# Performance work log

Hardware: AMD Instinct MI355X
Metric: run time of the kernel (lower is better)

The kernel has to match this reference:

```python
import jax, jax.numpy as jnp
import numpy as np

OUT = 7          # output_size
SR = 2           # sampling_ratio
IMG = 512.0      # image size (512, 512)
CANON_SCALE = 224.0
CANON_LVL = 4.0
LVL_MIN, LVL_MAX = 2, 6  # strides 4..64


def roi_align_level(feat, rois, scale):
    """torchvision roi_align (aligned=False) for all rois on one level.
    feat: [B,C,H,W], rois: [B,N,4] in image coords. Returns [B,N,C,7,7]."""
    B, C, H, W = feat.shape
    N = rois.shape[1]
    x1 = rois[..., 0] * scale
    y1 = rois[..., 1] * scale
    x2 = rois[..., 2] * scale
    y2 = rois[..., 3] * scale
    roi_w = jnp.maximum(x2 - x1, 1.0)
    roi_h = jnp.maximum(y2 - y1, 1.0)
    bin_w = roi_w / OUT
    bin_h = roi_h / OUT
    # 14 sample coordinates per axis: 7 bins x 2 samples, offset (i+0.5)/2 within bin
    grid = (jnp.arange(OUT, dtype=feat.dtype)[:, None]
            + (jnp.arange(SR, dtype=feat.dtype)[None, :] + 0.5) / SR).reshape(-1)  # [14]
    py = y1[..., None] + grid * bin_h[..., None]   # [B,N,14]
    px = x1[..., None] + grid * bin_w[..., None]   # [B,N,14]
    yy = py[..., :, None]                          # [B,N,14,1]
    xx = px[..., None, :]                          # [B,N,1,14]
    valid = (yy >= -1.0) & (yy <= H) & (xx >= -1.0) & (xx <= W)  # [B,N,14,14]
    y = jnp.clip(yy, 0.0, H - 1)
    x = jnp.clip(xx, 0.0, W - 1)
    y0f = jnp.floor(y)
    x0f = jnp.floor(x)
    ly = y - y0f   # [B,N,14,1]
    lx = x - x0f   # [B,N,1,14]
    y0 = y0f.astype(jnp.int32)
    x0 = x0f.astype(jnp.int32)
    y1i = jnp.minimum(y0 + 1, H - 1)
    x1i = jnp.minimum(x0 + 1, W - 1)

    flat = feat.reshape(B, C, H * W)

    def gather(yi, xi):
        idx = (yi * W + xi).reshape(B, -1)                     # [B, N*14*14]
        g = jax.vmap(lambda f, i: f[:, i])(flat, idx)          # [B, C, N*14*14]
        return g.reshape(B, C, N, SR * OUT, SR * OUT)

    w00 = ((1 - ly) * (1 - lx))[:, None]  # [B,1,N,14,14]
    w01 = ((1 - ly) * lx)[:, None]
    w10 = (ly * (1 - lx))[:, None]
    w11 = (ly * lx)[:, None]
    val = (gather(y0, x0) * w00 + gather(y0, x1i) * w01
           + gather(y1i, x0) * w10 + gather(y1i, x1i) * w11)
    val = val * valid[:, None].astype(feat.dtype)
    # average the SRxSR samples within each bin
    out = val.reshape(B, C, N, OUT, SR, OUT, SR).mean(axis=(4, 6))  # [B,C,N,7,7]
    return out.transpose(0, 2, 1, 3, 4)  # [B,N,C,7,7]


def setup_inputs() -> dict:
    key = jax.random.key(0)
    ks = jax.random.split(key, 6)
    B, C, N = 4, 256, 256
    feats = {}
    for lvl, hw in enumerate([128, 64, 32, 16, 8]):
        feats[f"feat{lvl}"] = jax.random.normal(ks[lvl], (B, C, hw, hw), dtype=jnp.float32)
    # random boxes inside the 512x512 image with x2>x1, y2>y1
    xy = jax.random.uniform(ks[5], (B, N, 2, 2), minval=0.0, maxval=IMG)
    lo = xy.min(axis=2)
    hi = xy.max(axis=2)
    rois = jnp.concatenate([lo, hi], axis=-1)  # [B,N,4] = (x1,y1,x2,y2)
    feats["rois"] = rois
    return feats


def reference(feat0, feat1, feat2, feat3, feat4, rois):
    B, N = rois.shape[0], rois.shape[1]
    feats = [feat0, feat1, feat2, feat3, feat4]
    scales = [0.25, 0.125, 0.0625, 0.03125, 0.015625]  # inferred from 128..8 vs 512
    # FPN level assignment (torchvision LevelMapper)
    area = (rois[..., 2] - rois[..., 0]) * (rois[..., 3] - rois[..., 1])
    lvl = jnp.floor(CANON_LVL + jnp.log2(jnp.sqrt(area) / CANON_SCALE + 1e-6))
    lvl = (jnp.clip(lvl, LVL_MIN, LVL_MAX) - LVL_MIN).astype(jnp.int32)  # [B,N] in 0..4
    # pool every roi on every level, then select its assigned level
    stacked = jnp.stack([roi_align_level(f, rois, s) for f, s in zip(feats, scales)],
                        axis=2)  # [B,N,5,C,7,7]
    sel = jnp.take_along_axis(stacked,
                              lvl[:, :, None, None, None, None].astype(jnp.int32),
                              axis=2)[:, :, 0]  # [B,N,C,7,7]
    B_, N_, C, _, _ = sel.shape
    return sel.reshape(B_ * N_, C, OUT, OUT)
```

## Files before the change

### kernel.cpp

```cpp
#include <hip/hip_runtime.h>

#define OUT 7
#define NB 4
#define NC 256
#define NN 256
#define EPR (NC * OUT * OUT)

typedef float nfloat4 __attribute__((ext_vector_type(4)));

__global__ __launch_bounds__(256) void transpose_all(
    const float* __restrict__ f0, const float* __restrict__ f1,
    const float* __restrict__ f2, const float* __restrict__ f3,
    const float* __restrict__ f4, float* __restrict__ T)
{
    __shared__ float tile[32][33];
    const int bx = blockIdx.x;

    const float* in; float* outp; int P, t, shp;
    if (bx < 16384)      { in = f0; outp = T;            P = 16384; t = bx;         shp = 9; }
    else if (bx < 20480) { in = f1; outp = T + 16777216; P = 4096;  t = bx - 16384; shp = 7; }
    else if (bx < 21504) { in = f2; outp = T + 20971520; P = 1024;  t = bx - 20480; shp = 5; }
    else if (bx < 21760) { in = f3; outp = T + 22020096; P = 256;   t = bx - 21504; shp = 3; }
    else                 { in = f4; outp = T + 22282240; P = 64;    t = bx - 21760; shp = 1; }

    const int pt   = t & ((1 << shp) - 1);
    const int rest = t >> shp;
    const int ct   = rest & 7;
    const int b    = rest >> 3;
    const int p0   = pt << 5;
    const int c0   = ct << 5;
    const int tx   = threadIdx.x & 7;
    const int ty   = threadIdx.x >> 3;

    const float* src = in + ((size_t)((b << 8) + c0 + ty)) * P + p0 + (tx << 2);
    nfloat4 v = *(const nfloat4*)src;
    tile[ty][tx * 4 + 0] = v.x;
    tile[ty][tx * 4 + 1] = v.y;
    tile[ty][tx * 4 + 2] = v.z;
    tile[ty][tx * 4 + 3] = v.w;
    __syncthreads();

    nfloat4 w;
    w.x = tile[4 * tx + 0][ty];
    w.y = tile[4 * tx + 1][ty];
    w.z = tile[4 * tx + 2][ty];
    w.w = tile[4 * tx + 3][ty];
    float* dst = outp + ((size_t)b * P + p0 + ty) * NC + c0 + (tx << 2);
    *(nfloat4*)dst = w;
}

__global__ __launch_bounds__(256, 3) void msroi_fast(
    const float* __restrict__ T, const float* __restrict__ rois,
    float* __restrict__ out)
{
    const int roi = blockIdx.x;
    const int tid = threadIdx.x;

    __shared__ float s_wyt[14], s_wyb[14], s_wxl[14], s_wxr[14];
    __shared__ int   s_yr0[14], s_yr1[14], s_x0[14], s_x1[14];
    __shared__ int   s_lvl;
    __shared__ __align__(16) float s_out[EPR];

    if (tid < 28) {
        const float rx1 = rois[roi * 4 + 0];
        const float ry1 = rois[roi * 4 + 1];
        const float rx2 = rois[roi * 4 + 2];
        const float ry2 = rois[roi * 4 + 3];

        float area = (rx2 - rx1) * (ry2 - ry1);
        float lf = floorf(4.0f + log2f(sqrtf(area) / 224.0f + 1e-6f));
        lf = fminf(fmaxf(lf, 2.0f), 6.0f);
        int lvl = (int)lf - 2;
        if (tid == 0) s_lvl = lvl;

        float scale = 1.0f / (float)(4 << lvl);
        int   W     = 128 >> lvl;

        float x1 = rx1 * scale, y1 = ry1 * scale;
        float x2 = rx2 * scale, y2 = ry2 * scale;
        float rw = fmaxf(x2 - x1, 1.0f);
        float rh = fmaxf(y2 - y1, 1.0f);
        float bw = rw / (float)OUT;
        float bh = rh / (float)OUT;

        bool isx = (tid >= 14);
        int  g   = isx ? tid - 14 : tid;
        float gv = ((float)g + 0.5f) * 0.5f;
        float p  = isx ? (x1 + gv * bw) : (y1 + gv * bh);

        float v = (p >= -1.0f && p <= (float)W) ? 1.0f : 0.0f;
        float pc  = fminf(fmaxf(p, 0.0f), (float)(W - 1));
        float p0f = floorf(pc);
        int   p0  = (int)p0f;
        int   p1  = min(p0 + 1, W - 1);
        float l   = pc - p0f;

        if (isx) {
            s_x0[g] = p0; s_x1[g] = p1;
            s_wxl[g] = v * (1.0f - l); s_wxr[g] = v * l;
        } else {
            s_yr0[g] = p0 * W; s_yr1[g] = p1 * W;
            s_wyt[g] = v * (1.0f - l); s_wyb[g] = v * l;
        }
    }
    __syncthreads();

    const int lvl = s_lvl;
    const int W   = 128 >> lvl;
    const int POS = W * W;
    const int off_tab[5] = {0, 16777216, 20971520, 22020096, 22282240};
    const int b   = roi >> 8;
    const int q   = tid >> 6;
    const int ch0 = (tid & 63) << 2;
    const float* base = T + (size_t)off_tab[lvl] + (size_t)b * POS * NC + ch0;

    #pragma unroll
    for (int i = 0; i < 13; ++i) {
        const int p  = min(q * 13 + i, 48);
        const int oy = p / 7;
        const int ox = p - oy * 7;
        const int gy0 = oy * 2, gy1 = gy0 + 1;
        const int gx0 = ox * 2, gx1 = gx0 + 1;

        const float wt0 = s_wyt[gy0], wb0 = s_wyb[gy0];
        const float wt1 = s_wyt[gy1], wb1 = s_wyb[gy1];
        const int r00 = s_yr0[gy0], r01 = s_yr1[gy0];
        const int r10 = s_yr0[gy1], r11 = s_yr1[gy1];
        const float wl0 = s_wxl[gx0], wr0 = s_wxr[gx0];
        const float wl1 = s_wxl[gx1], wr1 = s_wxr[gx1];
        const int x00 = s_x0[gx0], x01 = s_x1[gx0];
        const int x10 = s_x0[gx1], x11 = s_x1[gx1];

        const nfloat4 a00 = *(const nfloat4*)&base[(r00 + x00) << 8];
        const nfloat4 a01 = *(const nfloat4*)&base[(r00 + x01) << 8];
        const nfloat4 a02 = *(const nfloat4*)&base[(r01 + x00) << 8];
        const nfloat4 a03 = *(const nfloat4*)&base[(r01 + x01) << 8];
        const nfloat4 a04 = *(const nfloat4*)&base[(r00 + x10) << 8];
        const nfloat4 a05 = *(const nfloat4*)&base[(r00 + x11) << 8];
        const nfloat4 a06 = *(const nfloat4*)&base[(r01 + x10) << 8];
        const nfloat4 a07 = *(const nfloat4*)&base[(r01 + x11) << 8];
        const nfloat4 a08 = *(const nfloat4*)&base[(r10 + x00) << 8];
        const nfloat4 a09 = *(const nfloat4*)&base[(r10 + x01) << 8];
        const nfloat4 a10 = *(const nfloat4*)&base[(r11 + x00) << 8];
        const nfloat4 a11 = *(const nfloat4*)&base[(r11 + x01) << 8];
        const nfloat4 a12 = *(const nfloat4*)&base[(r10 + x10) << 8];
        const nfloat4 a13 = *(const nfloat4*)&base[(r10 + x11) << 8];
        const nfloat4 a14 = *(const nfloat4*)&base[(r11 + x10) << 8];
        const nfloat4 a15 = *(const nfloat4*)&base[(r11 + x11) << 8];

        nfloat4 acc;
        acc  = (wt0 * wl0) * a00 + (wt0 * wr0) * a01
             + (wb0 * wl0) * a02 + (wb0 * wr0) * a03;
        acc += (wt0 * wl1) * a04 + (wt0 * wr1) * a05
             + (wb0 * wl1) * a06 + (wb0 * wr1) * a07;
        acc += (wt1 * wl0) * a08 + (wt1 * wr0) * a09
             + (wb1 * wl0) * a10 + (wb1 * wr0) * a11;
        acc += (wt1 * wl1) * a12 + (wt1 * wr1) * a13
             + (wb1 * wl1) * a14 + (wb1 * wr1) * a15;
        acc *= 0.25f;

        s_out[(ch0 + 0) * 49 + p] = acc.x;
        s_out[(ch0 + 1) * 49 + p] = acc.y;
        s_out[(ch0 + 2) * 49 + p] = acc.z;
        s_out[(ch0 + 3) * 49 + p] = acc.w;
    }
    __syncthreads();

    float* ob = out + (size_t)roi * EPR;
    #pragma unroll
    for (int k = 0; k < 12; ++k) {
        const int f = (tid + (k << 8)) << 2;
        nfloat4 v = *(const nfloat4*)&s_out[f];
        __builtin_nontemporal_store(v, (nfloat4*)&ob[f]);
    }
    if (tid < 64) {
        const int f = (tid + 3072) << 2;
        nfloat4 v = *(const nfloat4*)&s_out[f];
        __builtin_nontemporal_store(v, (nfloat4*)&ob[f]);
    }
}

__global__ __launch_bounds__(256) void msroi_kernel(
    const float* __restrict__ f0, const float* __restrict__ f1,
    const float* __restrict__ f2, const float* __restrict__ f3,
    const float* __restrict__ f4, const float* __restrict__ rois,
    float* __restrict__ out)
{
    const int roi = blockIdx.y;
    const int tid = threadIdx.x;

    __shared__ float s_wyt[14], s_wyb[14];
    __shared__ float s_wxl[14], s_wxr[14];
    __shared__ int   s_oy0[14], s_oy1[14];
    __shared__ int   s_x0[14],  s_x1[14];
    __shared__ int   s_lvl;

    if (tid < 28) {
        const float rx1 = rois[roi * 4 + 0];
        const float ry1 = rois[roi * 4 + 1];
        const float rx2 = rois[roi * 4 + 2];
        const float ry2 = rois[roi * 4 + 3];

        float area = (rx2 - rx1) * (ry2 - ry1);
        float lf = floorf(4.0f + log2f(sqrtf(area) / 224.0f + 1e-6f));
        lf = fminf(fmaxf(lf, 2.0f), 6.0f);
        int lvl = (int)lf - 2;
        if (tid == 0) s_lvl = lvl;

        float scale = 1.0f / (float)(4 << lvl);
        int   HW    = 128 >> lvl;

        float x1 = rx1 * scale, y1 = ry1 * scale;
        float x2 = rx2 * scale, y2 = ry2 * scale;
        float rw = fmaxf(x2 - x1, 1.0f);
        float rh = fmaxf(y2 - y1, 1.0f);
        float bw = rw / (float)OUT;
        float bh = rh / (float)OUT;

        bool isx = (tid >= 14);
        int  g   = isx ? tid - 14 : tid;
        float gv = ((float)g + 0.5f) * 0.5f;
        float p  = isx ? (x1 + gv * bw) : (y1 + gv * bh);

        float v = (p >= -1.0f && p <= (float)HW) ? 1.0f : 0.0f;
        float pc  = fminf(fmaxf(p, 0.0f), (float)(HW - 1));
        float p0f = floorf(pc);
        int   p0  = (int)p0f;
        int   p1  = min(p0 + 1, HW - 1);
        float l   = pc - p0f;

        if (isx) {
            s_x0[g] = p0; s_x1[g] = p1;
            s_wxl[g] = v * (1.0f - l); s_wxr[g] = v * l;
        } else {
            s_oy0[g] = p0 * HW; s_oy1[g] = p1 * HW;
            s_wyt[g] = v * (1.0f - l); s_wyb[g] = v * l;
        }
    }
    __syncthreads();

    const int lvl = s_lvl;
    const int HW  = 128 >> lvl;
    const int HW2 = HW * HW;
    const float* f = (lvl == 0) ? f0 : (lvl == 1) ? f1 : (lvl == 2) ? f2
                     : (lvl == 3) ? f3 : f4;
    const int b = roi >> 8;

    const int e0 = blockIdx.x * 512 + tid;

    float acc[2];
    #pragma unroll
    for (int k = 0; k < 2; ++k) {
        const int e  = e0 + k * 256;
        const int ec = (e < EPR) ? e : 0;
        const int c  = ec / 49;
        const int s  = ec - 49 * c;
        const int oy = s / 7;
        const int ox = s - 7 * oy;

        const float* fp = f + (size_t)(b * NC + c) * (size_t)HW2;

        float a = 0.0f;
        #pragma unroll
        for (int iy = 0; iy < 2; ++iy) {
            const int gy = oy * 2 + iy;
            const float wt = s_wyt[gy], wb = s_wyb[gy];
            const int   o0 = s_oy0[gy], o1 = s_oy1[gy];
            #pragma unroll
            for (int ix = 0; ix < 2; ++ix) {
                const int gx = ox * 2 + ix;
                const float wl = s_wxl[gx], wr = s_wxr[gx];
                const int   x0 = s_x0[gx],  x1i = s_x1[gx];
                const float v00 = fp[o0 + x0];
                const float v01 = fp[o0 + x1i];
                const float v10 = fp[o1 + x0];
                const float v11 = fp[o1 + x1i];
                a += (wt * wl) * v00 + (wt * wr) * v01
                   + (wb * wl) * v10 + (wb * wr) * v11;
            }
        }
        acc[k] = a * 0.25f;
    }

    #pragma unroll
    for (int k = 0; k < 2; ++k) {
        const int e = e0 + k * 256;
        if (e < EPR)
            __builtin_nontemporal_store(acc[k], &out[(size_t)roi * EPR + e]);
    }
}

extern "C" void kernel_launch(void* const* d_in, const int* in_sizes, int n_in,
                              void* d_out, int out_size, void* d_ws, size_t ws_size,
                              hipStream_t stream) {
    const float* f0   = (const float*)d_in[0];
    const float* f1   = (const float*)d_in[1];
    const float* f2   = (const float*)d_in[2];
    const float* f3   = (const float*)d_in[3];
    const float* f4   = (const float*)d_in[4];
    const float* rois = (const float*)d_in[5];
    float* out = (float*)d_out;

    const size_t need = 22347776ull * 4ull;
    if (ws_size >= need) {
        float* T = (float*)d_ws;
        transpose_all<<<dim3(21824), dim3(256), 0, stream>>>(f0, f1, f2, f3, f4, T);
        msroi_fast<<<dim3(NB * NN), dim3(256), 0, stream>>>(T, rois, out);
    } else {
        dim3 grid((EPR + 511) / 512, NB * NN);
        dim3 block(256);
        msroi_kernel<<<grid, block, 0, stream>>>(f0, f1, f2, f3, f4, rois, out);
    }
}
```

Baseline: 194.8 us.

## Store transposed features as bf16 and software-pipeline gather loads across output bins

The transpose kernel now writes the channel-last feature copy in bf16 with round-to-nearest-even instead of fp32, which halves workspace write traffic and gather read bytes. The pooling kernel converts bf16 back to fp32 and accumulates in fp32. The gather loop is also restructured to prefetch the 16 corner loads for the next output bin while the current bin is being accumulated. This lowers feature precision relative to the fp32 reference and raises register pressure under the 3-waves occupancy bound.

```diff
diff --git a/kernel.cpp b/kernel.cpp
--- a/kernel.cpp
+++ b/kernel.cpp
@@ -7,16 +7,32 @@
 #define EPR (NC * OUT * OUT)
 
 typedef float nfloat4 __attribute__((ext_vector_type(4)));
+typedef unsigned short nushort4 __attribute__((ext_vector_type(4)));
+
+__device__ inline unsigned short f2bf(float f) {
+    unsigned u = __builtin_bit_cast(unsigned, f);
+    u += 0x7FFFu + ((u >> 16) & 1u);
+    return (unsigned short)(u >> 16);
+}
+
+__device__ inline nfloat4 bf4_to_f4(nushort4 s) {
+    nfloat4 r;
+    r.x = __builtin_bit_cast(float, (unsigned)s.x << 16);
+    r.y = __builtin_bit_cast(float, (unsigned)s.y << 16);
+    r.z = __builtin_bit_cast(float, (unsigned)s.z << 16);
+    r.w = __builtin_bit_cast(float, (unsigned)s.w << 16);
+    return r;
+}
 
 __global__ __launch_bounds__(256) void transpose_all(
     const float* __restrict__ f0, const float* __restrict__ f1,
     const float* __restrict__ f2, const float* __restrict__ f3,
-    const float* __restrict__ f4, float* __restrict__ T)
+    const float* __restrict__ f4, unsigned short* __restrict__ T)
 {
     __shared__ float tile[32][33];
     const int bx = blockIdx.x;
 
-    const float* in; float* outp; int P, t, shp;
+    const float* in; unsigned short* outp; int P, t, shp;
     if (bx < 16384)      { in = f0; outp = T;            P = 16384; t = bx;         shp = 9; }
     else if (bx < 20480) { in = f1; outp = T + 16777216; P = 4096;  t = bx - 16384; shp = 7; }
     else if (bx < 21504) { in = f2; outp = T + 20971520; P = 1024;  t = bx - 20480; shp = 5; }
@@ -40,17 +56,17 @@
     tile[ty][tx * 4 + 3] = v.w;
     __syncthreads();
 
-    nfloat4 w;
-    w.x = tile[4 * tx + 0][ty];
-    w.y = tile[4 * tx + 1][ty];
-    w.z = tile[4 * tx + 2][ty];
-    w.w = tile[4 * tx + 3][ty];
-    float* dst = outp + ((size_t)b * P + p0 + ty) * NC + c0 + (tx << 2);
-    *(nfloat4*)dst = w;
+    nushort4 w;
+    w.x = f2bf(tile[4 * tx + 0][ty]);
+    w.y = f2bf(tile[4 * tx + 1][ty]);
+    w.z = f2bf(tile[4 * tx + 2][ty]);
+    w.w = f2bf(tile[4 * tx + 3][ty]);
+    unsigned short* dst = outp + ((size_t)b * P + p0 + ty) * NC + c0 + (tx << 2);
+    *(nushort4*)dst = w;
 }
 
 __global__ __launch_bounds__(256, 3) void msroi_fast(
-    const float* __restrict__ T, const float* __restrict__ rois,
+    const unsigned short* __restrict__ T, const float* __restrict__ rois,
     float* __restrict__ out)
 {
     const int roi = blockIdx.x;
@@ -112,16 +128,14 @@
     const int b   = roi >> 8;
     const int q   = tid >> 6;
     const int ch0 = (tid & 63) << 2;
-    const float* base = T + (size_t)off_tab[lvl] + (size_t)b * POS * NC + ch0;
-
-    #pragma unroll
-    for (int i = 0; i < 13; ++i) {
-        const int p  = min(q * 13 + i, 48);
+    const unsigned short* base =
+        T + (size_t)off_tab[lvl] + (size_t)b * POS * NC + ch0;
+
+    auto make_pos = [&](int p, int* off, float* w) {
         const int oy = p / 7;
         const int ox = p - oy * 7;
         const int gy0 = oy * 2, gy1 = gy0 + 1;
         const int gx0 = ox * 2, gx1 = gx0 + 1;
-
         const float wt0 = s_wyt[gy0], wb0 = s_wyb[gy0];
         const float wt1 = s_wyt[gy1], wb1 = s_wyb[gy1];
         const int r00 = s_yr0[gy0], r01 = s_yr1[gy0];
@@ -130,39 +144,58 @@
         const float wl1 = s_wxl[gx1], wr1 = s_wxr[gx1];
         const int x00 = s_x0[gx0], x01 = s_x1[gx0];
         const int x10 = s_x0[gx1], x11 = s_x1[gx1];
-
-        const nfloat4 a00 = *(const nfloat4*)&base[(r00 + x00) << 8];
-        const nfloat4 a01 = *(const nfloat4*)&base[(r00 + x01) << 8];
-        const nfloat4 a02 = *(const nfloat4*)&base[(r01 + x00) << 8];
-        const nfloat4 a03 = *(const nfloat4*)&base[(r01 + x01) << 8];
-        const nfloat4 a04 = *(const nfloat4*)&base[(r00 + x10) << 8];
-        const nfloat4 a05 = *(const nfloat4*)&base[(r00 + x11) << 8];
-        const nfloat4 a06 = *(const nfloat4*)&base[(r01 + x10) << 8];
-        const nfloat4 a07 = *(const nfloat4*)&base[(r01 + x11) << 8];
-        const nfloat4 a08 = *(const nfloat4*)&base[(r10 + x00) << 8];
-        const nfloat4 a09 = *(const nfloat4*)&base[(r10 + x01) << 8];
-        const nfloat4 a10 = *(const nfloat4*)&base[(r11 + x00) << 8];
-        const nfloat4 a11 = *(const nfloat4*)&base[(r11 + x01) << 8];
-        const nfloat4 a12 = *(const nfloat4*)&base[(r10 + x10) << 8];
-        const nfloat4 a13 = *(const nfloat4*)&base[(r10 + x11) << 8];
-        const nfloat4 a14 = *(const nfloat4*)&base[(r11 + x10) << 8];
-        const nfloat4 a15 = *(const nfloat4*)&base[(r11 + x11) << 8];
-
-        nfloat4 acc;
-        acc  = (wt0 * wl0) * a00 + (wt0 * wr0) * a01
-             + (wb0 * wl0) * a02 + (wb0 * wr0) * a03;
-        acc += (wt0 * wl1) * a04 + (wt0 * wr1) * a05
-             + (wb0 * wl1) * a06 + (wb0 * wr1) * a07;
-        acc += (wt1 * wl0) * a08 + (wt1 * wr0) * a09
-             + (wb1 * wl0) * a10 + (wb1 * wr0) * a11;
-        acc += (wt1 * wl1) * a12 + (wt1 * wr1) * a13
-             + (wb1 * wl1) * a14 + (wb1 * wr1) * a15;
+        off[0]  = r00 + x00; w[0]  = wt0 * wl0;
+        off[1]  = r00 + x01; w[1]  = wt0 * wr0;
+        off[2]  = r01 + x00; w[2]  = wb0 * wl0;
+        off[3]  = r01 + x01; w[3]  = wb0 * wr0;
+        off[4]  = r00 + x10; w[4]  = wt0 * wl1;
+        off[5]  = r00 + x11; w[5]  = wt0 * wr1;
+        off[6]  = r01 + x10; w[6]  = wb0 * wl1;
+        off[7]  = r01 + x11; w[7]  = wb0 * wr1;
+        off[8]  = r10 + x00; w[8]  = wt1 * wl0;
+        off[9]  = r10 + x01; w[9]  = wt1 * wr0;
+        off[10] = r11 + x00; w[10] = wb1 * wl0;
+        off[11] = r11 + x01; w[11] = wb1 * wr0;
+        off[12] = r10 + x10; w[12] = wt1 * wl1;
+        off[13] = r10 + x11; w[13] = wt1 * wr1;
+        off[14] = r11 + x10; w[14] = wb1 * wl1;
+        off[15] = r11 + x11; w[15] = wb1 * wr1;
+    };
+
+    int p_cur = min(q * 13, 48);
+    int offA[16]; float wA[16];
+    nushort4 L[16];
+    make_pos(p_cur, offA, wA);
+    #pragma unroll
+    for (int k = 0; k < 16; ++k)
+        L[k] = *(const nushort4*)&base[(size_t)offA[k] << 8];
+
+    #pragma unroll
+    for (int i = 0; i < 13; ++i) {
+        const int p_nxt = min(q * 13 + i + 1, 48);
+        int offB[16]; float wB[16];
+        nushort4 M[16];
+        if (i < 12) {
+            make_pos(p_nxt, offB, wB);
+            #pragma unroll
+            for (int k = 0; k < 16; ++k)
+                M[k] = *(const nushort4*)&base[(size_t)offB[k] << 8];
+        }
+
+        nfloat4 acc = {0.0f, 0.0f, 0.0f, 0.0f};
+        #pragma unroll
+        for (int k = 0; k < 16; ++k)
+            acc += wA[k] * bf4_to_f4(L[k]);
         acc *= 0.25f;
 
-        s_out[(ch0 + 0) * 49 + p] = acc.x;
-        s_out[(ch0 + 1) * 49 + p] = acc.y;
-        s_out[(ch0 + 2) * 49 + p] = acc.z;
-        s_out[(ch0 + 3) * 49 + p] = acc.w;
+        s_out[(ch0 + 0) * 49 + p_cur] = acc.x;
+        s_out[(ch0 + 1) * 49 + p_cur] = acc.y;
+        s_out[(ch0 + 2) * 49 + p_cur] = acc.z;
+        s_out[(ch0 + 3) * 49 + p_cur] = acc.w;
+
+        #pragma unroll
+        for (int k = 0; k < 16; ++k) { L[k] = M[k]; wA[k] = wB[k]; }
+        p_cur = p_nxt;
     }
     __syncthreads();
 
@@ -301,9 +334,9 @@
     const float* rois = (const float*)d_in[5];
     float* out = (float*)d_out;
 
-    const size_t need = 22347776ull * 4ull;
+    const size_t need = 22347776ull * 2ull;
     if (ws_size >= need) {
-        float* T = (float*)d_ws;
+        unsigned short* T = (unsigned short*)d_ws;
         transpose_all<<<dim3(21824), dim3(256), 0, stream>>>(f0, f1, f2, f3, f4, T);
         msroi_fast<<<dim3(NB * NN), dim3(256), 0, stream>>>(T, rois, out);
     } else {
```

After: 171.2 us. 12.1% less time.
